# Kernel optimization log

Measured on AMD Instinct MI355X. Metric: run time of the kernel, lower is better.

## Reference

```python
import jax, jax.numpy as jnp
import numpy as np

CHAR_NUM = 5000
EMB = 128
RAD_EMB = 64
TOTAL_RAD = 300
HID = 512
CLS = 10
B, T = 64, 512
PAD_ID, START_ID, END_ID = 0, 8, 9
NEG = -10000.0


def setup_inputs() -> dict:
    key = jax.random.key(0)
    ks = jax.random.split(key, 16)
    s = 0.08
    D_in = EMB + RAD_EMB
    inp = {
        "batch_data": jax.random.randint(ks[0], (B, T), 0, CHAR_NUM, dtype=jnp.int32),
        "batch_onerad": jax.random.randint(ks[1], (B, T), 0, TOTAL_RAD, dtype=jnp.int32),
        "batch_tag": jax.random.randint(ks[2], (B, T), 0, START_ID, dtype=jnp.int32),
        "char_emb": jax.random.normal(ks[3], (CHAR_NUM, EMB), jnp.float32) * s,
        "rad_emb": jax.random.normal(ks[4], (TOTAL_RAD, RAD_EMB), jnp.float32) * s,
        "w_ih_f": jax.random.normal(ks[5], (4 * HID, D_in), jnp.float32) * s,
        "w_hh_f": jax.random.normal(ks[6], (4 * HID, HID), jnp.float32) * s,
        "b_f": jax.random.normal(ks[7], (4 * HID,), jnp.float32) * s,
        "w_ih_b": jax.random.normal(ks[8], (4 * HID, D_in), jnp.float32) * s,
        "w_hh_b": jax.random.normal(ks[9], (4 * HID, HID), jnp.float32) * s,
        "b_b": jax.random.normal(ks[10], (4 * HID,), jnp.float32) * s,
        "w_cls": jax.random.normal(ks[11], (CLS, 2 * HID), jnp.float32) * s,
        "b_cls": jax.random.normal(ks[12], (CLS,), jnp.float32) * s,
    }
    # transition[to, from] init per the module's __init__
    trans = np.full((CLS, CLS), 1.0 / CLS, dtype=np.float32)
    trans[START_ID, :] = NEG
    trans[:, END_ID] = NEG
    trans[PAD_ID, END_ID] = 0.05
    inp["transition"] = jnp.asarray(trans)
    return inp


def _run_lstm(xs, w_ih, w_hh, b):
    # xs: [T, B, D] -> hs: [T, B, H]; torch gate order i,f,g,o
    Bsz = xs.shape[1]
    h0 = jnp.zeros((Bsz, HID), xs.dtype)
    c0 = jnp.zeros((Bsz, HID), xs.dtype)

    def step(carry, x_t):
        h, c = carry
        g = x_t @ w_ih.T + h @ w_hh.T + b
        i, f, gg, o = jnp.split(g, 4, axis=-1)
        c = jax.nn.sigmoid(f) * c + jax.nn.sigmoid(i) * jnp.tanh(gg)
        h = jax.nn.sigmoid(o) * jnp.tanh(c)
        return (h, c), h

    _, hs = jax.lax.scan(step, (h0, c0), xs)
    return hs


def _emissions(batch_data, batch_onerad, char_emb, rad_emb,
               w_ih_f, w_hh_f, b_f, w_ih_b, w_hh_b, b_b, w_cls, b_cls):
    emb = jnp.concatenate([char_emb[batch_data], rad_emb[batch_onerad]], axis=2)  # [B,T,D]
    # dropout in eval mode == identity
    xs = jnp.transpose(emb, (1, 0, 2))  # [T,B,D]
    hs_f = _run_lstm(xs, w_ih_f, w_hh_f, b_f)
    hs_b = _run_lstm(xs[::-1], w_ih_b, w_hh_b, b_b)[::-1]
    hs = jnp.concatenate([hs_f, hs_b], axis=-1)  # [T,B,2H]
    emission = hs @ w_cls.T + b_cls  # [T,B,C]
    return jnp.transpose(emission, (1, 0, 2))  # [B,T,C]


def _forward_alg(feats, transition):
    # feats: [B,T,C]; CRF partition function per batch element
    Bsz, _, C = feats.shape
    alpha0 = jnp.full((C, Bsz), NEG, feats.dtype).at[START_ID, :].set(0.0)
    feats_t = jnp.transpose(feats, (1, 2, 0))  # [T, C(to), B]

    def step(alpha, feat_t):
        # aa[to, from, b]
        aa = alpha[None, :, :] + feat_t[:, None, :] + transition[:, :, None]
        return jax.nn.logsumexp(aa, axis=1), None

    alpha, _ = jax.lax.scan(step, alpha0, feats_t)
    return jax.nn.logsumexp(alpha, axis=0)  # [B]


def _score_sentence(feats, tags, transition):
    # feats: [B,T,C], tags: [B,T]
    Bsz = feats.shape[0]
    start = jnp.full((Bsz, 1), START_ID, tags.dtype)
    tags_ext = jnp.concatenate([start, tags], axis=1)  # [B,T+1]
    trans_sc = transition[tags_ext[:, 1:], tags_ext[:, :-1]].sum(axis=1)  # [B]
    emit_sc = jnp.take_along_axis(feats, tags[:, :, None], axis=2)[..., 0].sum(axis=1)
    return trans_sc + emit_sc  # [B]


def reference(batch_data, batch_onerad, batch_tag, char_emb, rad_emb,
              w_ih_f, w_hh_f, b_f, w_ih_b, w_hh_b, b_b, w_cls, b_cls, transition):
    feats = _emissions(batch_data, batch_onerad, char_emb, rad_emb,
                       w_ih_f, w_hh_f, b_f, w_ih_b, w_hh_b, b_b, w_cls, b_cls)
    fwd = _forward_alg(feats, transition)
    gold = _score_sentence(feats, batch_tag, transition)
    Bsz = feats.shape[0]
    loss = (fwd.sum() - gold.sum()) / Bsz
    return loss
```

## Files before the change

kernel.cpp:

```cpp
#include <hip/hip_runtime.h>

typedef unsigned short u16;
typedef unsigned int u32;
typedef float f32x16 __attribute__((ext_vector_type(16)));
typedef float f32x4v __attribute__((ext_vector_type(4)));
typedef unsigned int u32x4 __attribute__((ext_vector_type(4)));
typedef unsigned int u32x2 __attribute__((ext_vector_type(2)));

#define TT 512
#define NBLK 64

static const size_t OFF_EMBX = 0;
static const size_t OFF_HS   = 12582912;
static const size_t OFF_HBUF = 79691776;
static const size_t OFF_BAR  = 79953920;
static const size_t OFF_FEAT = 79954176;
static const size_t OFF_RES  = 81264896;
static const size_t WS_NEED  = 81265152;

__device__ inline u32 packbf(float a, float b) {
  u32 ua = __float_as_uint(a); ua += 0x7fffu + ((ua >> 16) & 1u);
  u32 ub = __float_as_uint(b); ub += 0x7fffu + ((ub >> 16) & 1u);
  return (ua >> 16) | (ub & 0xffff0000u);
}
__device__ inline u16 f2b(float a) {
  u32 u = __float_as_uint(a); u += 0x7fffu + ((u >> 16) & 1u);
  return (u16)(u >> 16);
}
__device__ inline float sigm(float x) { return 1.f / (1.f + __expf(-x)); }
__device__ inline float tanhx(float x) {
  float e = __expf(-2.f * fabsf(x));
  float t = (1.f - e) / (1.f + e);
  return (x < 0.f) ? -t : t;
}

__device__ inline u32x4 ldg_cc(const u16* p) {
  u32x4 r;
  asm volatile("global_load_dwordx4 %0, %1, off sc0 sc1"
               : "=v"(r) : "v"(p) : "memory");
  return r;
}
__device__ inline void stg_cc8(u16* p, u32x2 v) {
  asm volatile("global_store_dwordx2 %0, %1, off sc0 sc1"
               :: "v"(p), "v"(v) : "memory");
}
__device__ inline int ldflag(const int* p) {
  int r;
  asm volatile("global_load_dword %0, %1, off sc0 sc1"
               : "=v"(r) : "v"(p) : "memory");
  asm volatile("s_waitcnt vmcnt(0)" ::: "memory");
  return r;
}
__device__ inline void stflag(int* p, int v) {
  asm volatile("global_store_dword %0, %1, off sc0 sc1"
               :: "v"(p), "v"(v) : "memory");
}

__global__ __launch_bounds__(256) void k_embed(const int* __restrict__ bdata,
                                               const int* __restrict__ brad,
                                               const float* __restrict__ cemb,
                                               const float* __restrict__ remb,
                                               u16* __restrict__ embX) {
  int t = blockIdx.x;
  int tid = threadIdx.x;
#pragma unroll
  for (int r = 0; r < 6; ++r) {
    int cc = r * 256 + tid;
    int b = cc / 24;
    int j = cc - b * 24;
    int ic = bdata[b * TT + t];
    int ir = brad[b * TT + t];
    const float* src = (j < 16) ? (cemb + (size_t)ic * 128 + j * 8)
                                : (remb + (size_t)ir * 64 + (j - 16) * 8);
    f32x4v f0 = *(const f32x4v*)src;
    f32x4v f1 = *(const f32x4v*)(src + 4);
    u32x4 o;
    o[0] = packbf(f0[0], f0[1]); o[1] = packbf(f0[2], f0[3]);
    o[2] = packbf(f1[0], f1[1]); o[3] = packbf(f1[2], f1[3]);
    *(u32x4*)(embX + ((size_t)t * 64 + b) * 192 + j * 8) = o;
  }
}

__global__ __launch_bounds__(256, 1) void k_lstm(
    const u16* __restrict__ embX, u16* __restrict__ hbuf, u16* __restrict__ hs,
    const float* __restrict__ wihf, const float* __restrict__ whhf, const float* __restrict__ bf,
    const float* __restrict__ wihb, const float* __restrict__ whhb, const float* __restrict__ bb,
    int* __restrict__ flags) {
  __shared__ u16 smh[64 * 512];
  __shared__ float gl[64 * 68];

  const int tid = threadIdx.x;
  const int lane = tid & 63;
  const int wid = tid >> 6;
  const int blk = blockIdx.x;
  const int dir = blk >> 5;
  const int j0 = (blk & 31) << 4;

  const float* wih = dir ? wihb : wihf;
  const float* whh = dir ? whhb : whhf;
  const float* bias = dir ? bb : bf;

  const int m = wid >> 1, n = wid & 1;
  const int l31 = lane & 31;
  const int hi = lane >> 5;

  const int lr = m * 32 + l31;
  const int strip = lr >> 4, rr = lr & 15;
  const int grow = strip * 512 + j0 + rr;
  const float* pih = wih + (size_t)grow * 192 + 8 * hi;
  const float* phh = whh + (size_t)grow * 512 + 8 * hi;
  u32x4 aw[44];
#pragma unroll
  for (int kt = 0; kt < 44; ++kt) {
    const float* p = (kt < 12) ? (pih + kt * 16) : (phh + (kt - 12) * 16);
    f32x4v f0 = *(const f32x4v*)p;
    f32x4v f1 = *(const f32x4v*)(p + 4);
    u32x4 a;
    a[0] = packbf(f0[0], f0[1]); a[1] = packbf(f0[2], f0[3]);
    a[2] = packbf(f1[0], f1[1]); a[3] = packbf(f1[2], f1[3]);
    aw[kt] = a;
  }

  u16* hb_dT = hbuf + dir * 65536;

  const int bb_ = n * 32 + l31;
  const int swzr = (bb_ & 15) << 4;
  const char* hbase = (const char*)smh + bb_ * 1024;
  const int hoff = hi * 16;

  const int pb = tid >> 2;
  const int pj = (tid & 3) * 4;
  float creg[4] = {0.f, 0.f, 0.f, 0.f};
  float bI[4], bF[4], bG[4], bO[4];
#pragma unroll
  for (int q = 0; q < 4; ++q) {
    bI[q] = bias[j0 + pj + q];
    bF[q] = bias[512 + j0 + pj + q];
    bG[q] = bias[1024 + j0 + pj + q];
    bO[q] = bias[1536 + j0 + pj + q];
  }

  int* myflags = flags + dir * 64;

  for (int t = 0; t < TT; ++t) {
    const int par = t & 1;
    const int tx = dir ? (511 - t) : t;

    u32x4 xf[12];
    const u16* xbase = embX + ((size_t)tx * 64 + bb_) * 192 + 8 * hi;
#pragma unroll
    for (int kt = 0; kt < 12; ++kt) xf[kt] = *(const u32x4*)(xbase + kt * 16);

    if (t) {
      int f = ldflag(myflags + (lane & 31) * 2);
      int guard = 0;
      while (__any(f < t)) {
        if (++guard > 300000) break;
        __builtin_amdgcn_s_sleep(1);
        f = ldflag(myflags + (lane & 31) * 2);
      }
    }

    {
      const u16* src = hb_dT + par * 32768;
#pragma unroll
      for (int half = 0; half < 2; ++half) {
        u32x4 v[8];
#pragma unroll
        for (int r = 0; r < 8; ++r) {
          int b = (half * 8 + r) * 4 + wid;
          v[r] = ldg_cc(src + b * 512 + lane * 8);
        }
        asm volatile("s_waitcnt vmcnt(0)" ::: "memory");
#pragma unroll
        for (int r = 0; r < 8; ++r) {
          int b = (half * 8 + r) * 4 + wid;
          int kk = (lane * 8) ^ ((b & 15) << 3);
          *(u32x4*)(smh + b * 512 + kk) = v[r];
        }
      }
    }
    __syncthreads();

    f32x16 acc;
#pragma unroll
    for (int i = 0; i < 16; ++i) acc[i] = 0.f;
    asm volatile("s_nop 7\ns_nop 7");
#pragma unroll
    for (int kt = 0; kt < 32; ++kt) {
      u32x4 bfrag = *(const u32x4*)(hbase + ((kt * 32 + hoff) ^ swzr));
      asm("v_mfma_f32_32x32x16_bf16 %0, %1, %2, %0" : "+v"(acc) : "v"(aw[kt]), "v"(bfrag));
    }
#pragma unroll
    for (int kt = 0; kt < 12; ++kt) {
      asm("v_mfma_f32_32x32x16_bf16 %0, %1, %2, %0" : "+v"(acc) : "v"(aw[32 + kt]), "v"(xf[kt]));
    }
    asm volatile("s_nop 7\ns_nop 7\ns_nop 7");

#pragma unroll
    for (int r = 0; r < 16; ++r) {
      int row = (r & 3) + 8 * (r >> 2) + 4 * hi;
      gl[(m * 32 + row) * 68 + (n * 32 + l31)] = acc[r];
    }
    __syncthreads();

    {
      u16* dstT = hb_dT + (par ^ 1) * 32768;
      u32 hp0 = 0, hp1 = 0;
#pragma unroll
      for (int q = 0; q < 4; ++q) {
        int j = pj + q;
        float gi = gl[j * 68 + pb] + bI[q];
        float gf = gl[(16 + j) * 68 + pb] + bF[q];
        float gg = gl[(32 + j) * 68 + pb] + bG[q];
        float go = gl[(48 + j) * 68 + pb] + bO[q];
        float cn = sigm(gf) * creg[q] + sigm(gi) * tanhx(gg);
        creg[q] = cn;
        float h = sigm(go) * tanhx(cn);
        u32 h16 = (u32)f2b(h);
        if (q == 0) hp0 = h16;
        else if (q == 1) hp0 |= h16 << 16;
        else if (q == 2) hp1 = h16;
        else hp1 |= h16 << 16;
      }
      u32x2 hv; hv[0] = hp0; hv[1] = hp1;
      stg_cc8(dstT + pb * 512 + j0 + pj, hv);
      *(u32x2*)(hs + ((size_t)tx * 64 + pb) * 1024 + dir * 512 + j0 + pj) = hv;
    }

    if (t != TT - 1) {
      asm volatile("s_waitcnt vmcnt(0)" ::: "memory");
      __syncthreads();
      if (tid == 0) stflag(myflags + (blk & 31) * 2, t + 1);
    }
  }
}

__global__ __launch_bounds__(256) void k_emis(const u16* __restrict__ hs,
                                              const float* __restrict__ wcls,
                                              const float* __restrict__ bcls,
                                              float* __restrict__ feats) {
  __shared__ float wl[10240];
  int tid = threadIdx.x;
  for (int i = tid; i < 10240; i += 256) wl[i] = wcls[i];
  __syncthreads();
  int row = blockIdx.x * 256 + tid;
  const u16* hrow = hs + (size_t)row * 1024;
  float acc[10];
#pragma unroll
  for (int c = 0; c < 10; ++c) acc[c] = bcls[c];
  for (int k0 = 0; k0 < 1024; k0 += 8) {
    u32x4 v = *(const u32x4*)(hrow + k0);
    float x0 = __uint_as_float(v[0] << 16);
    float x1 = __uint_as_float(v[0] & 0xffff0000u);
    float x2 = __uint_as_float(v[1] << 16);
    float x3 = __uint_as_float(v[1] & 0xffff0000u);
    float x4 = __uint_as_float(v[2] << 16);
    float x5 = __uint_as_float(v[2] & 0xffff0000u);
    float x6 = __uint_as_float(v[3] << 16);
    float x7 = __uint_as_float(v[3] & 0xffff0000u);
#pragma unroll
    for (int c = 0; c < 10; ++c) {
      const float* w = &wl[c * 1024 + k0];
      f32x4v wa = *(const f32x4v*)w;
      f32x4v wb = *(const f32x4v*)(w + 4);
      acc[c] += x0 * wa[0] + x1 * wa[1] + x2 * wa[2] + x3 * wa[3] +
                x4 * wb[0] + x5 * wb[1] + x6 * wb[2] + x7 * wb[3];
    }
  }
#pragma unroll
  for (int c = 0; c < 10; ++c) feats[(size_t)row * 10 + c] = acc[c];
}

__global__ void k_crf(const float* __restrict__ feats, const float* __restrict__ trans,
                      const int* __restrict__ btag, float* __restrict__ res) {
  int b = blockIdx.x;
  int lane = threadIdx.x;
  float tr[10];
  int to = lane < 10 ? lane : 9;
#pragma unroll
  for (int f = 0; f < 10; ++f) tr[f] = trans[to * 10 + f];
  float al[10];
#pragma unroll
  for (int f = 0; f < 10; ++f) al[f] = (f == 8) ? 0.f : -10000.f;
  float fe_next = (lane < 10) ? feats[(size_t)b * 10 + lane] : 0.f;
  for (int t = 0; t < 512; ++t) {
    float fe = fe_next;
    if (t < 511)
      fe_next = (lane < 10) ? feats[((size_t)(t + 1) * 64 + b) * 10 + lane] : 0.f;
    float mx = -3.0e38f;
#pragma unroll
    for (int f = 0; f < 10; ++f) mx = fmaxf(mx, al[f] + tr[f]);
    float s = 0.f;
#pragma unroll
    for (int f = 0; f < 10; ++f) s += __expf(al[f] + tr[f] - mx);
    float an = mx + __logf(s) + fe;
#pragma unroll
    for (int f = 0; f < 10; ++f) al[f] = __shfl(an, f);
  }
  float mx = -3.0e38f;
#pragma unroll
  for (int f = 0; f < 10; ++f) mx = fmaxf(mx, al[f]);
  float s = 0.f;
#pragma unroll
  for (int f = 0; f < 10; ++f) s += __expf(al[f] - mx);
  float fwd = mx + __logf(s);
  float g = 0.f;
  for (int t = lane; t < 512; t += 64) {
    int tg = btag[b * 512 + t];
    int pv = (t == 0) ? 8 : btag[b * 512 + t - 1];
    g += trans[tg * 10 + pv] + feats[((size_t)t * 64 + b) * 10 + tg];
  }
#pragma unroll
  for (int off = 32; off > 0; off >>= 1) g += __shfl_down(g, off);
  if (lane == 0) res[b] = fwd - g;
}

__global__ void k_fin(const float* __restrict__ res, float* __restrict__ out) {
  float v = res[threadIdx.x];
#pragma unroll
  for (int off = 32; off > 0; off >>= 1) v += __shfl_down(v, off);
  if (threadIdx.x == 0) out[0] = v * (1.f / 64.f);
}

extern "C" void kernel_launch(void* const* d_in, const int* in_sizes, int n_in,
                              void* d_out, int out_size, void* d_ws, size_t ws_size,
                              hipStream_t stream) {
  (void)in_sizes; (void)n_in; (void)out_size;
  if (ws_size < WS_NEED) return;

  const int* bdata = (const int*)d_in[0];
  const int* brad  = (const int*)d_in[1];
  const int* btag  = (const int*)d_in[2];
  const float* cemb = (const float*)d_in[3];
  const float* remb = (const float*)d_in[4];
  const float* wihf = (const float*)d_in[5];
  const float* whhf = (const float*)d_in[6];
  const float* bf   = (const float*)d_in[7];
  const float* wihb = (const float*)d_in[8];
  const float* whhb = (const float*)d_in[9];
  const float* bb   = (const float*)d_in[10];
  const float* wcls = (const float*)d_in[11];
  const float* bcls = (const float*)d_in[12];
  const float* trans = (const float*)d_in[13];

  char* ws = (char*)d_ws;
  u16* embX = (u16*)(ws + OFF_EMBX);
  u16* hs   = (u16*)(ws + OFF_HS);
  u16* hbuf = (u16*)(ws + OFF_HBUF);
  int* flags = (int*)(ws + OFF_BAR);
  float* feats = (float*)(ws + OFF_FEAT);
  float* res = (float*)(ws + OFF_RES);

  hipMemsetAsync(ws + OFF_HBUF, 0, 262144 + 512, stream);

  k_embed<<<512, 256, 0, stream>>>(bdata, brad, cemb, remb, embX);
  k_lstm<<<64, 256, 0, stream>>>(embX, hbuf, hs, wihf, whhf, bf, wihb, whhb, bb, flags);
  k_emis<<<128, 256, 0, stream>>>(hs, wcls, bcls, feats);
  k_crf<<<64, 64, 0, stream>>>(feats, trans, btag, res);
  k_fin<<<1, 64, 0, stream>>>(res, (float*)d_out);
}
```

Before: 3.218 ms.

## Permute LSTM weight rows so gate math runs directly on MFMA accumulators

Reorders the A-operand weight rows so that each lane's 32x32 MFMA accumulator holds the i/f/g/o gates for the same hidden units. The cell update can then read them straight from registers, which removes the LDS gate staging buffer and one block barrier per timestep. The change also merges the two halves of the hidden-state load into a single batch of 16 outstanding loads, and drops the sleep from the flag spin loop while lowering its guard bound. These cut per-step latency on the serial recurrence, at the cost of more register pressure and busier polling of the flags.

```diff
diff --git a/kernel.cpp b/kernel.cpp
--- a/kernel.cpp
+++ b/kernel.cpp
@@ -87,7 +87,6 @@
     const float* __restrict__ wihb, const float* __restrict__ whhb, const float* __restrict__ bb,
     int* __restrict__ flags) {
   __shared__ u16 smh[64 * 512];
-  __shared__ float gl[64 * 68];
 
   const int tid = threadIdx.x;
   const int lane = tid & 63;
@@ -104,9 +103,9 @@
   const int l31 = lane & 31;
   const int hi = lane >> 5;
 
-  const int lr = m * 32 + l31;
-  const int strip = lr >> 4, rr = lr & 15;
-  const int grow = strip * 512 + j0 + rr;
+  const int gate = l31 >> 3;
+  const int jloc = (l31 & 7) + 8 * m;
+  const int grow = gate * 512 + j0 + jloc;
   const float* pih = wih + (size_t)grow * 192 + 8 * hi;
   const float* phh = whh + (size_t)grow * 512 + 8 * hi;
   u32x4 aw[44];
@@ -128,16 +127,15 @@
   const char* hbase = (const char*)smh + bb_ * 1024;
   const int hoff = hi * 16;
 
-  const int pb = tid >> 2;
-  const int pj = (tid & 3) * 4;
+  const int jme = j0 + 8 * m + 4 * hi;
   float creg[4] = {0.f, 0.f, 0.f, 0.f};
   float bI[4], bF[4], bG[4], bO[4];
 #pragma unroll
   for (int q = 0; q < 4; ++q) {
-    bI[q] = bias[j0 + pj + q];
-    bF[q] = bias[512 + j0 + pj + q];
-    bG[q] = bias[1024 + j0 + pj + q];
-    bO[q] = bias[1536 + j0 + pj + q];
+    bI[q] = bias[jme + q];
+    bF[q] = bias[512 + jme + q];
+    bG[q] = bias[1024 + jme + q];
+    bO[q] = bias[1536 + jme + q];
   }
 
   int* myflags = flags + dir * 64;
@@ -155,29 +153,25 @@
       int f = ldflag(myflags + (lane & 31) * 2);
       int guard = 0;
       while (__any(f < t)) {
-        if (++guard > 300000) break;
-        __builtin_amdgcn_s_sleep(1);
+        if (++guard > 20000) break;
         f = ldflag(myflags + (lane & 31) * 2);
       }
     }
 
     {
       const u16* src = hb_dT + par * 32768;
-#pragma unroll
-      for (int half = 0; half < 2; ++half) {
-        u32x4 v[8];
-#pragma unroll
-        for (int r = 0; r < 8; ++r) {
-          int b = (half * 8 + r) * 4 + wid;
-          v[r] = ldg_cc(src + b * 512 + lane * 8);
-        }
-        asm volatile("s_waitcnt vmcnt(0)" ::: "memory");
-#pragma unroll
-        for (int r = 0; r < 8; ++r) {
-          int b = (half * 8 + r) * 4 + wid;
-          int kk = (lane * 8) ^ ((b & 15) << 3);
-          *(u32x4*)(smh + b * 512 + kk) = v[r];
-        }
+      u32x4 v[16];
+#pragma unroll
+      for (int r = 0; r < 16; ++r) {
+        int b = r * 4 + wid;
+        v[r] = ldg_cc(src + b * 512 + lane * 8);
+      }
+      asm volatile("s_waitcnt vmcnt(0)" ::: "memory");
+#pragma unroll
+      for (int r = 0; r < 16; ++r) {
+        int b = r * 4 + wid;
+        int kk = (lane * 8) ^ ((b & 15) << 3);
+        *(u32x4*)(smh + b * 512 + kk) = v[r];
       }
     }
     __syncthreads();
@@ -197,23 +191,15 @@
     }
     asm volatile("s_nop 7\ns_nop 7\ns_nop 7");
 
-#pragma unroll
-    for (int r = 0; r < 16; ++r) {
-      int row = (r & 3) + 8 * (r >> 2) + 4 * hi;
-      gl[(m * 32 + row) * 68 + (n * 32 + l31)] = acc[r];
-    }
-    __syncthreads();
-
     {
       u16* dstT = hb_dT + (par ^ 1) * 32768;
       u32 hp0 = 0, hp1 = 0;
 #pragma unroll
       for (int q = 0; q < 4; ++q) {
-        int j = pj + q;
-        float gi = gl[j * 68 + pb] + bI[q];
-        float gf = gl[(16 + j) * 68 + pb] + bF[q];
-        float gg = gl[(32 + j) * 68 + pb] + bG[q];
-        float go = gl[(48 + j) * 68 + pb] + bO[q];
+        float gi = acc[q] + bI[q];
+        float gf = acc[4 + q] + bF[q];
+        float gg = acc[8 + q] + bG[q];
+        float go = acc[12 + q] + bO[q];
         float cn = sigm(gf) * creg[q] + sigm(gi) * tanhx(gg);
         creg[q] = cn;
         float h = sigm(go) * tanhx(cn);
@@ -224,8 +210,8 @@
         else hp1 |= h16 << 16;
       }
       u32x2 hv; hv[0] = hp0; hv[1] = hp1;
-      stg_cc8(dstT + pb * 512 + j0 + pj, hv);
-      *(u32x2*)(hs + ((size_t)tx * 64 + pb) * 1024 + dir * 512 + j0 + pj) = hv;
+      stg_cc8(dstT + bb_ * 512 + jme, hv);
+      *(u32x2*)(hs + ((size_t)tx * 64 + bb_) * 1024 + dir * 512 + jme) = hv;
     }
 
     if (t != TT - 1) {
```

New measurement: 2.818 ms. 1.14x faster.
